# Kernel optimization log

Measured on AMD Instinct MI355X. Metric: run time of the kernel, lower is better.

## Reference

```python
import jax, jax.numpy as jnp
import numpy as np

W = 131072          # window size (number of observed frames)
J = 21              # number of joints
B = J - 1           # number of bones
F, PX, PY = 512.0, 512.0, 288.0   # pinhole intrinsics (SIZE_X=1024, SIZE_Y=576)
EPS = 1e-8
WEIGHTS = {"proj": 0.25, "lift": 0.25, "bone": 0.25, "smooth": 0.25}


def _euler_batch(roll, pitch, yaw):
    """Vectorized ZYX euler -> rotation matrices, numpy, [N,3,3]."""
    cr, sr = np.cos(roll), np.sin(roll)
    cp, sp = np.cos(pitch), np.sin(pitch)
    cy, sy = np.cos(yaw), np.sin(yaw)
    R = np.empty(roll.shape + (3, 3), np.float32)
    R[..., 0, 0] = cy * cp; R[..., 0, 1] = cy * sp * sr - sy * cr; R[..., 0, 2] = cy * sp * cr + sy * sr
    R[..., 1, 0] = sy * cp; R[..., 1, 1] = sy * sp * sr + cy * cr; R[..., 1, 2] = sy * sp * cr - cy * sr
    R[..., 2, 0] = -sp;     R[..., 2, 1] = cp * sr;                R[..., 2, 2] = cp * cr
    return R


def setup_inputs() -> dict:
    key = jax.random.key(0)
    ks = jax.random.split(key, 7)
    pose3d = jax.random.normal(ks[0], (W + 1, 3, J), jnp.float32)
    bone_2d = jax.random.normal(ks[1], (W, 2, J), jnp.float32)
    lift_dirs = jax.random.normal(ks[2], (W, 3, B), jnp.float32)
    # small proper drone rotations so the projection depth stays well away from 0
    ang = 0.05 * np.asarray(jax.random.normal(ks[3], (W, 3)))
    R_drone = jnp.asarray(_euler_batch(ang[:, 0], ang[:, 1], ang[:, 2]))
    # drone positions offset so pose - C_drone ~ +10 in every coordinate
    C_drone = 0.1 * jax.random.normal(ks[4], (W, 3, 1), jnp.float32) - 10.0
    bone_lengths = jax.random.uniform(ks[5], (B,), jnp.float32, 0.5, 1.5)
    R_cam = jnp.asarray(_euler_batch(np.zeros(1), np.full(1, np.pi / 2), np.zeros(1))[0])
    # chain skeleton: bone i connects joint i+1 -> joint i
    bone_connections = jnp.stack([jnp.arange(1, J, dtype=jnp.int32),
                                  jnp.arange(0, J - 1, dtype=jnp.int32)], axis=1)
    return {"pose3d": pose3d, "bone_2d": bone_2d, "lift_dirs": lift_dirs,
            "R_drone": R_drone, "C_drone": C_drone, "bone_lengths": bone_lengths,
            "R_cam": R_cam, "bone_connections": bone_connections}


def _forward(pose3d, bone_2d, lift_dirs, R_drone, C_drone, bone_lengths, R_cam,
             bone_connections):
    Jn = pose3d.shape[2]
    b0 = bone_connections[:, 0]
    b1 = bone_connections[:, 1]
    p = pose3d[1:]                                   # [W,3,J] frames with observations

    # ---- projection loss: cam = R_cam @ R_drone^T @ (p - C_drone), pinhole
    rel = p - C_drone                                # [W,3,J]
    cam = jnp.einsum('ij,wkj,wkn->win', R_cam, R_drone, rel)  # [W,3,J]
    z = cam[:, 2]
    proj2d = jnp.stack([F * cam[:, 0] / z + PX,
                        F * cam[:, 1] / z + PY], axis=1)       # [W,2,J]
    proj_loss = jnp.sum((proj2d - bone_2d) ** 2) / (2 * Jn)

    # ---- lift loss: unit bone direction vectors vs lifted directions
    bv = p[:, :, b0] - p[:, :, b1]                   # [W,3,B]
    dirs = bv / (jnp.linalg.norm(bv, axis=1, keepdims=True) + EPS)
    lift_loss = jnp.sum((lift_dirs - dirs) ** 2) / (3 * Jn)

    # ---- bone-length loss over all W+1 frames (squared lengths, as in torch code)
    bvall = pose3d[:, :, b0] - pose3d[:, :, b1]      # [W+1,3,B]
    blen = jnp.sum(bvall ** 2, axis=1)               # [W+1,B]
    bone_loss = jnp.sum((bone_lengths[None, :] - blen) ** 2) / (Jn - 1)

    # ---- smoothness: second difference of the pose trajectory
    d = pose3d[1:] - pose3d[:-1]                     # [W,3,J]
    smooth_loss = jnp.sum((d[1:] - d[:-1]) ** 2) / (3 * Jn)

    return (WEIGHTS["proj"] * proj_loss + WEIGHTS["lift"] * lift_loss
            + WEIGHTS["bone"] * bone_loss + WEIGHTS["smooth"] * smooth_loss)


def reference(pose3d, bone_2d, lift_dirs, R_drone, C_drone, bone_lengths, R_cam,
              bone_connections):
    return _forward(pose3d, bone_2d, lift_dirs, R_drone, C_drone, bone_lengths,
                    R_cam, bone_connections)
```

## Files before the change

kernel.cpp:

```cpp
#include <hip/hip_runtime.h>

namespace {

constexpr int JN = 21;
constexpr int BN = 20;
constexpr int FR = 64;
constexpr int HT = 32;
constexpr int SPLIT0 = 36;

constexpr float F_F  = 512.0f;
constexpr float PX_F = 512.0f;
constexpr float PY_F = 288.0f;
constexpr float EPS_F = 1e-8f;

constexpr float WPROJ   = 0.25f / (2.0f * 21.0f);
constexpr float WLIFT   = 0.25f / (3.0f * 21.0f);
constexpr float WBONE   = 0.25f / 20.0f;
constexpr float WSMOOTH = 0.25f / (3.0f * 21.0f);

__device__ __forceinline__ double block_reduce(double val) {
    __shared__ double smem[16];
    const int lane = threadIdx.x & 63;
    const int wid  = threadIdx.x >> 6;
    #pragma unroll
    for (int off = 32; off > 0; off >>= 1)
        val += __shfl_down(val, off, 64);
    if (lane == 0) smem[wid] = val;
    __syncthreads();
    if (wid == 0) {
        const int nw = blockDim.x >> 6;
        val = (lane < nw) ? smem[lane] : 0.0;
        #pragma unroll
        for (int off = 32; off > 0; off >>= 1)
            val += __shfl_down(val, off, 64);
    }
    return val;
}

__global__ __launch_bounds__(256) void pose_loss_kernel(
    const float* __restrict__ pose3d,
    const float* __restrict__ bone_2d,
    const float* __restrict__ lift_dirs,
    const float* __restrict__ R_drone,
    const float* __restrict__ C_drone,
    const float* __restrict__ bone_len,
    const float* __restrict__ R_cam,
    float* __restrict__ partials,
    int W)
{
    __shared__ alignas(16) float s_pose[(FR + 2) * 63 + 2];
    __shared__ alignas(16) float s_M[FR * 9];
    __shared__ alignas(16) float s_MC[FR * 3];

    const int tid = threadIdx.x;
    const int w0  = blockIdx.x * FR;
    const int nF  = min(FR, W - w0);
    const int nPoseF = min(FR + 2, W + 1 - w0);

    auto stage4 = [&](float* dst, const float* src, int nfl) {
        const int n4 = nfl >> 2;
        const float4* s4 = (const float4*)src;
        float4* d4 = (float4*)dst;
        for (int i = tid; i < n4; i += 256) d4[i] = s4[i];
        for (int i = (n4 << 2) + tid; i < nfl; i += 256) dst[i] = src[i];
    };

    auto computeM = [&](int base) {
        const int f = base + tid;
        if (tid < HT && f < nF) {
            const float* Rd = R_drone + (size_t)(w0 + f) * 9;
            float rd[9];
            #pragma unroll
            for (int k = 0; k < 9; ++k) rd[k] = Rd[k];
            float rc[9];
            #pragma unroll
            for (int k = 0; k < 9; ++k) rc[k] = R_cam[k];
            float M[9];
            #pragma unroll
            for (int i = 0; i < 3; ++i)
                #pragma unroll
                for (int k = 0; k < 3; ++k)
                    M[i * 3 + k] = rc[i * 3 + 0] * rd[k * 3 + 0]
                                 + rc[i * 3 + 1] * rd[k * 3 + 1]
                                 + rc[i * 3 + 2] * rd[k * 3 + 2];
            const float* Cp = C_drone + (size_t)(w0 + f) * 3;
            const float C0 = Cp[0], C1 = Cp[1], C2 = Cp[2];
            #pragma unroll
            for (int k = 0; k < 9; ++k) s_M[f * 9 + k] = M[k];
            #pragma unroll
            for (int i = 0; i < 3; ++i)
                s_MC[f * 3 + i] = M[i * 3 + 0] * C0 + M[i * 3 + 1] * C1 + M[i * 3 + 2] * C2;
        }
    };

    float partial = 0.0f;

    auto item = [&](int wl, int j) {
        const int w = w0 + wl;

        const float* P1 = s_pose + (wl + 1) * 63;
        const float p1x = P1[j];
        const float p1y = P1[JN + j];
        const float p1z = P1[2 * JN + j];

        {
            const float* M  = s_M  + wl * 9;
            const float* MC = s_MC + wl * 3;
            const float c0 = M[0] * p1x + M[1] * p1y + M[2] * p1z - MC[0];
            const float c1 = M[3] * p1x + M[4] * p1y + M[5] * p1z - MC[1];
            const float c2 = M[6] * p1x + M[7] * p1y + M[8] * p1z - MC[2];
            const float invz = 1.0f / c2;
            const float u = F_F * c0 * invz + PX_F;
            const float v = F_F * c1 * invz + PY_F;
            const float du = u - bone_2d[(size_t)w * 42 + j];
            const float dv = v - bone_2d[(size_t)w * 42 + JN + j];
            partial += WPROJ * (du * du + dv * dv);
        }

        if (j < BN) {
            const int b0 = j + 1;
            const int b1 = j;
            {
                const float ax = P1[b0]          - P1[b1];
                const float ay = P1[JN + b0]     - P1[JN + b1];
                const float az = P1[2 * JN + b0] - P1[2 * JN + b1];
                const float inv = 1.0f / (sqrtf(ax * ax + ay * ay + az * az) + EPS_F);
                const float lx = lift_dirs[(size_t)w * 60 + j]          - ax * inv;
                const float ly = lift_dirs[(size_t)w * 60 + BN + j]     - ay * inv;
                const float lz = lift_dirs[(size_t)w * 60 + 2 * BN + j] - az * inv;
                partial += WLIFT * (lx * lx + ly * ly + lz * lz);
            }
            const float blj = bone_len[j];
            {
                const float* P0 = s_pose + wl * 63;
                const float bx = P0[b0]          - P0[b1];
                const float by = P0[JN + b0]     - P0[JN + b1];
                const float bz = P0[2 * JN + b0] - P0[2 * JN + b1];
                const float bl = bx * bx + by * by + bz * bz;
                const float e = blj - bl;
                partial += WBONE * (e * e);
            }
            if (w == W - 1) {
                const float bx = P1[b0]          - P1[b1];
                const float by = P1[JN + b0]     - P1[JN + b1];
                const float bz = P1[2 * JN + b0] - P1[2 * JN + b1];
                const float bl = bx * bx + by * by + bz * bz;
                const float e = blj - bl;
                partial += WBONE * (e * e);
            }
        }

        if (w < W - 1) {
            const float* P0 = s_pose + wl * 63;
            const float* P2 = s_pose + (wl + 2) * 63;
            const float sx = P2[j]          - 2.0f * p1x + P0[j];
            const float sy = P2[JN + j]     - 2.0f * p1y + P0[JN + j];
            const float sz = P2[2 * JN + j] - 2.0f * p1z + P0[2 * JN + j];
            partial += WSMOOTH * (sx * sx + sy * sy + sz * sz);
        }
    };

    {
        const int f1 = min(SPLIT0, nPoseF);
        stage4(s_pose, pose3d + (size_t)w0 * 63, f1 * 63);
        computeM(0);
    }
    __syncthreads();

    if (nPoseF > SPLIT0) {
        stage4(s_pose + SPLIT0 * 63, pose3d + ((size_t)w0 + SPLIT0) * 63,
               (nPoseF - SPLIT0) * 63);
    }
    computeM(HT);

    {
        const int nItems0 = min(HT, nF) * JN;
        for (int it = tid; it < nItems0; it += 256) {
            const int wl = it / JN;
            const int j  = it - wl * JN;
            item(wl, j);
        }
    }
    __syncthreads();

    if (nF > HT) {
        const int nItems1 = (nF - HT) * JN;
        for (int it = tid; it < nItems1; it += 256) {
            const int wl = HT + it / JN;
            const int j  = it - (it / JN) * JN;
            item(wl, j);
        }
    }

    const double bsum = block_reduce((double)partial);
    if (tid == 0) partials[blockIdx.x] = (float)bsum;
}

__global__ __launch_bounds__(256) void final_reduce_kernel(
    const float* __restrict__ partials, float* __restrict__ out, int n)
{
    double v = 0.0;
    for (int i = threadIdx.x; i < n; i += blockDim.x)
        v += (double)partials[i];
    v = block_reduce(v);
    if (threadIdx.x == 0) out[0] = (float)v;
}

}

extern "C" void kernel_launch(void* const* d_in, const int* in_sizes, int n_in,
                              void* d_out, int out_size, void* d_ws, size_t ws_size,
                              hipStream_t stream) {
    const float* pose3d    = (const float*)d_in[0];
    const float* bone_2d   = (const float*)d_in[1];
    const float* lift_dirs = (const float*)d_in[2];
    const float* R_drone   = (const float*)d_in[3];
    const float* C_drone   = (const float*)d_in[4];
    const float* bone_len  = (const float*)d_in[5];
    const float* R_cam     = (const float*)d_in[6];
    float* out = (float*)d_out;
    float* partials = (float*)d_ws;

    const int W = in_sizes[3] / 9;
    const int grid = (W + FR - 1) / FR;

    pose_loss_kernel<<<grid, 256, 0, stream>>>(
        pose3d, bone_2d, lift_dirs, R_drone, C_drone, bone_len, R_cam, partials, W);
    final_reduce_kernel<<<1, 256, 0, stream>>>(partials, out, grid);
}
```

Measured before the change: 27.16 us.

## Fuse final reduction into main kernel via last-block atomic counter

Replaces the separate final-reduce kernel launch with a last-block-done pattern: each block stores its partial with release semantics, bumps a global atomic counter, and the last block sums all partials. A memset of the counter is added before launch. Also packs the per-frame rotation matrix and offset into a 12-float stride so they can be read as three float4 loads from shared memory. This trades a kernel launch for a memset plus atomics and serialised tail work in one block.

```diff
diff --git a/kernel.cpp b/kernel.cpp
--- a/kernel.cpp
+++ b/kernel.cpp
@@ -46,11 +46,13 @@
     const float* __restrict__ bone_len,
     const float* __restrict__ R_cam,
     float* __restrict__ partials,
+    unsigned int* __restrict__ counter,
+    float* __restrict__ out,
     int W)
 {
     __shared__ alignas(16) float s_pose[(FR + 2) * 63 + 2];
-    __shared__ alignas(16) float s_M[FR * 9];
-    __shared__ alignas(16) float s_MC[FR * 3];
+    __shared__ alignas(16) float s_M[FR * 12];
+    __shared__ unsigned int s_isLast;
 
     const int tid = threadIdx.x;
     const int w0  = blockIdx.x * FR;
@@ -86,10 +88,11 @@
             const float* Cp = C_drone + (size_t)(w0 + f) * 3;
             const float C0 = Cp[0], C1 = Cp[1], C2 = Cp[2];
             #pragma unroll
-            for (int k = 0; k < 9; ++k) s_M[f * 9 + k] = M[k];
+            for (int k = 0; k < 9; ++k) s_M[f * 12 + k] = M[k];
             #pragma unroll
             for (int i = 0; i < 3; ++i)
-                s_MC[f * 3 + i] = M[i * 3 + 0] * C0 + M[i * 3 + 1] * C1 + M[i * 3 + 2] * C2;
+                s_M[f * 12 + 9 + i] =
+                    M[i * 3 + 0] * C0 + M[i * 3 + 1] * C1 + M[i * 3 + 2] * C2;
         }
     };
 
@@ -104,11 +107,12 @@
         const float p1z = P1[2 * JN + j];
 
         {
-            const float* M  = s_M  + wl * 9;
-            const float* MC = s_MC + wl * 3;
-            const float c0 = M[0] * p1x + M[1] * p1y + M[2] * p1z - MC[0];
-            const float c1 = M[3] * p1x + M[4] * p1y + M[5] * p1z - MC[1];
-            const float c2 = M[6] * p1x + M[7] * p1y + M[8] * p1z - MC[2];
+            const float4 m0 = *(const float4*)(s_M + wl * 12);
+            const float4 m1 = *(const float4*)(s_M + wl * 12 + 4);
+            const float4 m2 = *(const float4*)(s_M + wl * 12 + 8);
+            const float c0 = m0.x * p1x + m0.y * p1y + m0.z * p1z - m2.y;
+            const float c1 = m0.w * p1x + m1.x * p1y + m1.y * p1z - m2.z;
+            const float c2 = m1.z * p1x + m1.w * p1y + m2.x * p1z - m2.w;
             const float invz = 1.0f / c2;
             const float u = F_F * c0 * invz + PX_F;
             const float v = F_F * c1 * invz + PY_F;
@@ -193,17 +197,23 @@
     }
 
     const double bsum = block_reduce((double)partial);
-    if (tid == 0) partials[blockIdx.x] = (float)bsum;
-}
-
-__global__ __launch_bounds__(256) void final_reduce_kernel(
-    const float* __restrict__ partials, float* __restrict__ out, int n)
-{
-    double v = 0.0;
-    for (int i = threadIdx.x; i < n; i += blockDim.x)
-        v += (double)partials[i];
-    v = block_reduce(v);
-    if (threadIdx.x == 0) out[0] = (float)v;
+
+    if (tid == 0) {
+        __hip_atomic_store(&partials[blockIdx.x], (float)bsum,
+                           __ATOMIC_RELEASE, __HIP_MEMORY_SCOPE_AGENT);
+        const unsigned int c = __hip_atomic_fetch_add(counter, 1u,
+                           __ATOMIC_ACQ_REL, __HIP_MEMORY_SCOPE_AGENT);
+        s_isLast = (c == gridDim.x - 1) ? 1u : 0u;
+    }
+    __syncthreads();
+    if (s_isLast) {
+        double v = 0.0;
+        for (int i = tid; i < (int)gridDim.x; i += 256)
+            v += (double)__hip_atomic_load(&partials[i],
+                           __ATOMIC_ACQUIRE, __HIP_MEMORY_SCOPE_AGENT);
+        v = block_reduce(v);
+        if (tid == 0) out[0] = (float)v;
+    }
 }
 
 }
@@ -219,12 +229,17 @@
     const float* bone_len  = (const float*)d_in[5];
     const float* R_cam     = (const float*)d_in[6];
     float* out = (float*)d_out;
-    float* partials = (float*)d_ws;
 
     const int W = in_sizes[3] / 9;
     const int grid = (W + FR - 1) / FR;
 
+    float* partials = (float*)d_ws;
+    unsigned int* counter =
+        (unsigned int*)((char*)d_ws + (((size_t)grid * 4 + 255) / 256) * 256);
+
+    hipMemsetAsync(counter, 0, sizeof(unsigned int), stream);
+
     pose_loss_kernel<<<grid, 256, 0, stream>>>(
-        pose3d, bone_2d, lift_dirs, R_drone, C_drone, bone_len, R_cam, partials, W);
-    final_reduce_kernel<<<1, 256, 0, stream>>>(partials, out, grid);
-}
+        pose3d, bone_2d, lift_dirs, R_drone, C_drone, bone_len, R_cam,
+        partials, counter, out, W);
+}
```

Measured after the change: 101.1 us. 3.72x slower.
